# Kernel tuning notes

Measured on AMD Instinct MI355X. Metric: run time of the kernel, lower is better.

## Reference

```python
import jax, jax.numpy as jnp
import numpy as np

N_NODES = 100000
N_EDGES = 1600000
IN_DIM, HIDDEN, OUT_DIM = 128, 64, 32
LN_EPS = 1e-5


def setup_inputs() -> dict:
    key = jax.random.key(0)
    ks = jax.random.split(key, 12)
    x = jax.random.normal(ks[0], (N_NODES, IN_DIM), dtype=jnp.float32)
    edge_index = jax.random.randint(ks[1], (2, N_EDGES), 0, N_NODES, dtype=jnp.int64)
    s = 1.0 / np.sqrt(IN_DIM)
    s2 = 1.0 / np.sqrt(HIDDEN)
    return {
        "x": x,
        "edge_index": edge_index,
        "W_self0": jax.random.uniform(ks[2], (IN_DIM, HIDDEN), jnp.float32, -s, s),
        "W_neigh0": jax.random.uniform(ks[3], (IN_DIM, HIDDEN), jnp.float32, -s, s),
        "b0": jnp.zeros((HIDDEN,), jnp.float32),
        "g0": jnp.ones((HIDDEN,), jnp.float32),
        "be0": jnp.zeros((HIDDEN,), jnp.float32),
        "W_self1": jax.random.uniform(ks[4], (HIDDEN, OUT_DIM), jnp.float32, -s2, s2),
        "W_neigh1": jax.random.uniform(ks[5], (HIDDEN, OUT_DIM), jnp.float32, -s2, s2),
        "b1": jnp.zeros((OUT_DIM,), jnp.float32),
        "g1": jnp.ones((OUT_DIM,), jnp.float32),
        "be1": jnp.zeros((OUT_DIM,), jnp.float32),
    }


def _sage_layer(h, src, dst, W_self, W_neigh, b, g, be):
    n = h.shape[0]
    # mean aggregation of neighbor features via scatter-add + count
    agg = jax.ops.segment_sum(h[src], dst, num_segments=n)  # [N, F]
    cnt = jax.ops.segment_sum(jnp.ones((src.shape[0],), h.dtype), dst, num_segments=n)
    agg = agg / jnp.clip(cnt, 1.0)[:, None]
    z = h @ W_self + agg @ W_neigh + b  # [N, out]
    mu = jnp.mean(z, axis=-1, keepdims=True)
    var = jnp.mean((z - mu) ** 2, axis=-1, keepdims=True)
    zn = (z - mu) * jax.lax.rsqrt(var + LN_EPS) * g + be
    return jax.nn.relu(zn)


def reference(x, edge_index, W_self0, W_neigh0, b0, g0, be0,
              W_self1, W_neigh1, b1, g1, be1):
    src, dst = edge_index[0], edge_index[1]
    h = _sage_layer(x, src, dst, W_self0, W_neigh0, b0, g0, be0)
    h = _sage_layer(h, src, dst, W_self1, W_neigh1, b1, g1, be1)
    return h
```

## Files before the change

kernel.cpp:

```cpp
#include <hip/hip_runtime.h>
#include <hip/hip_bf16.h>

#define N_NODES 100000
#define N_EDGES 1600000
#define IN_DIM 128
#define HID 64
#define OUT_DIM 32
#define LN_EPS 1e-5f
#define NBKT 782
#define NPBLK 500
#define PAIRS_PER_BLK 1600
#define G0BLK 1563

typedef __attribute__((ext_vector_type(8))) _Float16 half8;
typedef __attribute__((ext_vector_type(4))) float f32x4;

__device__ __forceinline__ float uf(unsigned short u) {
  return __uint_as_float(((unsigned int)u) << 16);
}
__device__ __forceinline__ float uflo(unsigned int u) {
  return __uint_as_float(u << 16);
}
__device__ __forceinline__ float ufhi(unsigned int u) {
  return __uint_as_float(u & 0xffff0000u);
}
__device__ __forceinline__ unsigned short bf16rne(float f) {
  unsigned int u = __float_as_uint(f);
  unsigned int r = u + 0x7fffu + ((u >> 16) & 1u);
  return (unsigned short)(r >> 16);
}

__global__ void detect_edges(const int* __restrict__ w, int* __restrict__ flag) {
  __shared__ int any;
  if (threadIdx.x == 0) any = 0;
  __syncthreads();
  if (w[2 * threadIdx.x + 1] != 0) any = 1;
  __syncthreads();
  if (threadIdx.x == 0) flag[0] = any ? 0 : 1;
}

__global__ __launch_bounds__(256) void convW(
    const float* __restrict__ Wn0, const float* __restrict__ Ws0,
    const float* __restrict__ Wn1, const float* __restrict__ Ws1,
    _Float16* __restrict__ B0f, _Float16* __restrict__ B1f) {
  const int i = blockIdx.x * 256 + threadIdx.x;
  if (i < 128 * 128) {
    const int n = i >> 7, k = i & 127;
    const float w = (n < 64) ? Wn0[k * 64 + n] : Ws0[k * 64 + (n - 64)];
    B0f[i] = (_Float16)w;
  } else if (i < 128 * 128 + 64 * 64) {
    const int j = i - 128 * 128;
    const int n = j >> 6, k = j & 63;
    const float w = (n < 32) ? Wn1[k * 32 + n] : Ws1[k * 32 + (n - 32)];
    B1f[j] = (_Float16)w;
  }
}

__global__ __launch_bounds__(256) void g0pc(
    const float* __restrict__ x, const _Float16* __restrict__ B0f,
    const float* __restrict__ b0,
    unsigned short* __restrict__ p0u, float* __restrict__ s0b,
    const int* __restrict__ w, const int* __restrict__ flag,
    int* __restrict__ gcount, int* __restrict__ blkbase) {
  __shared__ _Float16 lb[128 * 128];
  const int tid = threadIdx.x;

  if (blockIdx.x < NPBLK) {
    int* h = (int*)lb;
    const int b = blockIdx.x;
    for (int i = tid; i < NBKT; i += 256) h[i] = 0;
    __syncthreads();
    const int i64 = flag[0];
    const int pEnd = (b + 1) * PAIRS_PER_BLK;
    for (int p = b * PAIRS_PER_BLK + tid; p < pEnd; p += 256) {
      int d0, d1;
      if (i64) {
        const int4 vd = *(const int4*)(w + 2 * (size_t)N_EDGES + 4 * (size_t)p);
        d0 = vd.x; d1 = vd.z;
      } else {
        const int2 vd = *(const int2*)(w + (size_t)N_EDGES + 2 * (size_t)p);
        d0 = vd.x; d1 = vd.y;
      }
      atomicAdd(&h[d0 >> 7], 1);
      atomicAdd(&h[d1 >> 7], 1);
    }
    __syncthreads();
    for (int i = tid; i < NBKT; i += 256)
      blkbase[b * NBKT + i] = atomicAdd(&gcount[i], h[i]);
    return;
  }

  {
    const uint4* gb = (const uint4*)B0f;
    for (int i = tid; i < 2048; i += 256) {
      const int o = i << 4;
      const int sw = o ^ (((o >> 8) & 7) << 4);
      *(uint4*)((char*)lb + sw) = gb[i];
    }
  }
  __syncthreads();
  const int lane = tid & 63;
  const int wave = tid >> 6;
  const int rowbase = (blockIdx.x - NPBLK) * 64 + wave * 16;
  const int arow = rowbase + (lane & 15);
  const int rclamp = (arow < N_NODES) ? arow : 0;
  const int ko = (lane >> 4) << 3;

  f32x4 acc[8];
#pragma unroll
  for (int ct = 0; ct < 8; ++ct) acc[ct] = (f32x4){0.f, 0.f, 0.f, 0.f};

  for (int ks = 0; ks < 4; ++ks) {
    float av[8];
    const float* ax = x + (size_t)rclamp * IN_DIM + ks * 32 + ko;
    *(float4*)&av[0] = *(const float4*)ax;
    *(float4*)&av[4] = *(const float4*)(ax + 4);
    half8 ah;
#pragma unroll
    for (int j = 0; j < 8; ++j) ah[j] = (_Float16)av[j];
    const int kb = ks * 64 + (ko << 1);
#pragma unroll
    for (int ct = 0; ct < 8; ++ct) {
      const int n = ct * 16 + (lane & 15);
      const int boff = (n << 8) + kb;
      const int sb = boff ^ (((boff >> 8) & 7) << 4);
      const half8 bv = *(const half8*)((const char*)lb + sb);
      acc[ct] = __builtin_amdgcn_mfma_f32_16x16x32_f16(ah, bv, acc[ct], 0, 0, 0);
    }
  }
  const int rb4 = rowbase + ((lane >> 4) << 2);
  const int cc = lane & 15;
#pragma unroll
  for (int ct = 0; ct < 4; ++ct) {
#pragma unroll
    for (int j = 0; j < 4; ++j) {
      const int r = rb4 + j;
      if (r < N_NODES) p0u[(size_t)r * HID + ct * 16 + cc] = bf16rne(acc[ct][j]);
    }
  }
#pragma unroll
  for (int ct = 4; ct < 8; ++ct) {
    const float bias = b0[(ct - 4) * 16 + cc];
#pragma unroll
    for (int j = 0; j < 4; ++j) {
      const int r = rb4 + j;
      if (r < N_NODES) s0b[(size_t)r * HID + (ct - 4) * 16 + cc] = acc[ct][j] + bias;
    }
  }
}

__global__ __launch_bounds__(256) void part_scan(
    const int* __restrict__ gcount, int* __restrict__ gbase) {
  __shared__ int lds[256];
  const int t = threadIdx.x;
  int v[4];
  int s = 0;
#pragma unroll
  for (int j = 0; j < 4; ++j) {
    const int idx = t * 4 + j;
    v[j] = (idx < NBKT) ? gcount[idx] : 0;
    s += v[j];
  }
  lds[t] = s;
  __syncthreads();
  for (int o = 1; o < 256; o <<= 1) {
    const int val = (t >= o) ? lds[t - o] : 0;
    __syncthreads();
    lds[t] += val;
    __syncthreads();
  }
  int run = lds[t] - s;
#pragma unroll
  for (int j = 0; j < 4; ++j) {
    const int idx = t * 4 + j;
    if (idx < NBKT) gbase[idx] = run;
    run += v[j];
  }
}

__global__ __launch_bounds__(256) void part_scatter(
    const int* __restrict__ w, const int* __restrict__ flag,
    const int* __restrict__ gbase, const int* __restrict__ blkbase,
    int2* __restrict__ pe) {
  __shared__ int cur[NBKT];
  const int t = threadIdx.x, b = blockIdx.x;
  for (int i = t; i < NBKT; i += 256)
    cur[i] = gbase[i] + blkbase[b * NBKT + i];
  __syncthreads();
  const int i64 = flag[0];
  const int pEnd = (b + 1) * PAIRS_PER_BLK;
  for (int p = b * PAIRS_PER_BLK + t; p < pEnd; p += 256) {
    int s0, s1, d0, d1;
    if (i64) {
      const int4 vs = *(const int4*)(w + 4 * (size_t)p);
      const int4 vd = *(const int4*)(w + 2 * (size_t)N_EDGES + 4 * (size_t)p);
      s0 = vs.x; s1 = vs.z;
      d0 = vd.x; d1 = vd.z;
    } else {
      const int2 vs = *(const int2*)(w + 2 * (size_t)p);
      const int2 vd = *(const int2*)(w + (size_t)N_EDGES + 2 * (size_t)p);
      s0 = vs.x; s1 = vs.y;
      d0 = vd.x; d1 = vd.y;
    }
    const int sl0 = atomicAdd(&cur[d0 >> 7], 1);
    pe[sl0] = make_int2(s0, d0);
    const int sl1 = atomicAdd(&cur[d1 >> 7], 1);
    pe[sl1] = make_int2(s1, d1);
  }
}

__global__ __launch_bounds__(256) void bucket_csr(
    const int2* __restrict__ pe, const int* __restrict__ gbase,
    const int* __restrict__ gcount, int* __restrict__ deg,
    int* __restrict__ off, int* __restrict__ sortedSrc) {
  __shared__ int ldeg[128];
  __shared__ int loff[128];
  __shared__ int lcur[128];
  const int t = threadIdx.x;
  const int bkt = blockIdx.x;
  const int nbase = bkt << 7;
  const int ebase = gbase[bkt];
  const int cnt = gcount[bkt];
  if (t < 128) ldeg[t] = 0;
  __syncthreads();
  for (int e = t; e < cnt; e += 256) {
    const int2 sd = pe[ebase + e];
    atomicAdd(&ldeg[sd.y - nbase], 1);
  }
  __syncthreads();
  if (t < 128) loff[t] = ldeg[t];
  __syncthreads();
  for (int o = 1; o < 128; o <<= 1) {
    int v = 0;
    if (t >= o && t < 128) v = loff[t - o];
    __syncthreads();
    if (t < 128) loff[t] += v;
    __syncthreads();
  }
  if (t < 128) {
    const int ex = loff[t] - ldeg[t];
    lcur[t] = ex;
    const int n = nbase + t;
    if (n < N_NODES) {
      deg[n] = ldeg[t];
      off[n] = ebase + ex;
    }
  }
  __syncthreads();
  for (int e = t; e < cnt; e += 256) {
    const int2 sd = pe[ebase + e];
    const int p = atomicAdd(&lcur[sd.y - nbase], 1);
    sortedSrc[ebase + p] = sd.x;
  }
}

__global__ __launch_bounds__(256) void gemm1(
    const float* __restrict__ h1, const _Float16* __restrict__ B1f,
    const float* __restrict__ b1,
    unsigned short* __restrict__ p1u, float* __restrict__ s1b) {
  __shared__ _Float16 lb[64 * 64];
  const int tid = threadIdx.x;
  {
    const uint4* gb = (const uint4*)B1f;
    for (int i = tid; i < 512; i += 256) {
      const int o = i << 4;
      const int sw = o ^ (((o >> 7) & 7) << 4);
      *(uint4*)((char*)lb + sw) = gb[i];
    }
  }
  __syncthreads();
  const int lane = tid & 63;
  const int wave = tid >> 6;
  const int rowbase = blockIdx.x * 64 + wave * 16;
  const int arow = rowbase + (lane & 15);
  const int rclamp = (arow < N_NODES) ? arow : 0;
  const int ko = (lane >> 4) << 3;

  f32x4 acc[4];
#pragma unroll
  for (int ct = 0; ct < 4; ++ct) acc[ct] = (f32x4){0.f, 0.f, 0.f, 0.f};

  for (int ks = 0; ks < 2; ++ks) {
    float av[8];
    const float* ax = h1 + (size_t)rclamp * HID + ks * 32 + ko;
    *(float4*)&av[0] = *(const float4*)ax;
    *(float4*)&av[4] = *(const float4*)(ax + 4);
    half8 ah;
#pragma unroll
    for (int j = 0; j < 8; ++j) ah[j] = (_Float16)av[j];
    const int kb = ks * 64 + (ko << 1);
#pragma unroll
    for (int ct = 0; ct < 4; ++ct) {
      const int n = ct * 16 + (lane & 15);
      const int boff = (n << 7) + kb;
      const int sb = boff ^ (((boff >> 7) & 7) << 4);
      const half8 bv = *(const half8*)((const char*)lb + sb);
      acc[ct] = __builtin_amdgcn_mfma_f32_16x16x32_f16(ah, bv, acc[ct], 0, 0, 0);
    }
  }
  const int rb4 = rowbase + ((lane >> 4) << 2);
  const int cc = lane & 15;
#pragma unroll
  for (int ct = 0; ct < 2; ++ct) {
#pragma unroll
    for (int j = 0; j < 4; ++j) {
      const int r = rb4 + j;
      if (r < N_NODES) p1u[(size_t)r * OUT_DIM + ct * 16 + cc] = bf16rne(acc[ct][j]);
    }
  }
#pragma unroll
  for (int ct = 2; ct < 4; ++ct) {
    const float bias = b1[(ct - 2) * 16 + cc];
#pragma unroll
    for (int j = 0; j < 4; ++j) {
      const int r = rb4 + j;
      if (r < N_NODES)
        s1b[(size_t)r * OUT_DIM + (ct - 2) * 16 + cc] = acc[ct][j] + bias;
    }
  }
}

__global__ __launch_bounds__(256) void aggc0(
    const int* __restrict__ sortedSrc, const int* __restrict__ off,
    const int* __restrict__ deg, const unsigned short* __restrict__ p0u,
    const float* __restrict__ s0b, const float* __restrict__ g,
    const float* __restrict__ be, float* __restrict__ h1) {
  const int lane = threadIdx.x & 63;
  const int h = lane >> 5;
  const int grp = (lane >> 3) & 3;
  const int sl = lane & 7;
  const int i = blockIdx.x * 8 + ((threadIdx.x >> 6) << 1) + h;
  const int st = off[i];
  const int dg = deg[i];
  const int dgmax = max(dg, __shfl_xor(dg, 32));
  float acc[8];
#pragma unroll
  for (int f = 0; f < 8; ++f) acc[f] = 0.f;

  for (int base = 0; base < dgmax; base += 32) {
    const int cnt = min(32, dg - base);
    const int l5 = lane & 31;
    const int idx = (l5 < cnt) ? sortedSrc[st + base + l5] : 0;
    const int cntmax = min(32, dgmax - base);
    for (int j = 0; j * 4 < cntmax; ++j) {
      const int e = j * 4 + grp;
      const float msk = (e < cnt) ? 1.f : 0.f;
      const int es = max(min(e, cnt - 1), 0);
      const int srcn = __shfl(idx, (h << 5) | es);
      const uint4 q = *(const uint4*)(p0u + (size_t)srcn * HID + sl * 8);
      acc[0] = fmaf(msk, uflo(q.x), acc[0]);
      acc[1] = fmaf(msk, ufhi(q.x), acc[1]);
      acc[2] = fmaf(msk, uflo(q.y), acc[2]);
      acc[3] = fmaf(msk, ufhi(q.y), acc[3]);
      acc[4] = fmaf(msk, uflo(q.z), acc[4]);
      acc[5] = fmaf(msk, ufhi(q.z), acc[5]);
      acc[6] = fmaf(msk, uflo(q.w), acc[6]);
      acc[7] = fmaf(msk, ufhi(q.w), acc[7]);
    }
  }
#pragma unroll
  for (int mk = 8; mk < 32; mk <<= 1) {
#pragma unroll
    for (int f = 0; f < 8; ++f) acc[f] += __shfl_xor(acc[f], mk);
  }
  const float inv = 1.0f / fmaxf((float)dg, 1.0f);
  float z[8];
  const float4 sb0 = *(const float4*)(s0b + (size_t)i * HID + sl * 8);
  const float4 sb1 = *(const float4*)(s0b + (size_t)i * HID + sl * 8 + 4);
  z[0] = sb0.x + acc[0] * inv; z[1] = sb0.y + acc[1] * inv;
  z[2] = sb0.z + acc[2] * inv; z[3] = sb0.w + acc[3] * inv;
  z[4] = sb1.x + acc[4] * inv; z[5] = sb1.y + acc[5] * inv;
  z[6] = sb1.z + acc[6] * inv; z[7] = sb1.w + acc[7] * inv;
  float pm = 0.f;
#pragma unroll
  for (int f = 0; f < 8; ++f) pm += z[f];
#pragma unroll
  for (int mk = 1; mk < 8; mk <<= 1) pm += __shfl_xor(pm, mk);
  const float mean = pm * (1.0f / 64.0f);
  float pv = 0.f;
#pragma unroll
  for (int f = 0; f < 8; ++f) {
    z[f] -= mean;
    pv += z[f] * z[f];
  }
#pragma unroll
  for (int mk = 1; mk < 8; mk <<= 1) pv += __shfl_xor(pv, mk);
  const float rstd = rsqrtf(pv * (1.0f / 64.0f) + LN_EPS);
  if (grp == 0) {
    const float4 gv0 = *(const float4*)(g + sl * 8);
    const float4 gv1 = *(const float4*)(g + sl * 8 + 4);
    const float4 bv0 = *(const float4*)(be + sl * 8);
    const float4 bv1 = *(const float4*)(be + sl * 8 + 4);
    float4 o0, o1;
    o0.x = fmaxf(z[0] * rstd * gv0.x + bv0.x, 0.f);
    o0.y = fmaxf(z[1] * rstd * gv0.y + bv0.y, 0.f);
    o0.z = fmaxf(z[2] * rstd * gv0.z + bv0.z, 0.f);
    o0.w = fmaxf(z[3] * rstd * gv0.w + bv0.w, 0.f);
    o1.x = fmaxf(z[4] * rstd * gv1.x + bv1.x, 0.f);
    o1.y = fmaxf(z[5] * rstd * gv1.y + bv1.y, 0.f);
    o1.z = fmaxf(z[6] * rstd * gv1.z + bv1.z, 0.f);
    o1.w = fmaxf(z[7] * rstd * gv1.w + bv1.w, 0.f);
    *(float4*)(h1 + (size_t)i * HID + sl * 8) = o0;
    *(float4*)(h1 + (size_t)i * HID + sl * 8 + 4) = o1;
  }
}

__global__ __launch_bounds__(256) void aggc1(
    const int* __restrict__ sortedSrc, const int* __restrict__ off,
    const int* __restrict__ deg, const unsigned short* __restrict__ p1u,
    const float* __restrict__ s1b, const float* __restrict__ g,
    const float* __restrict__ be, float* __restrict__ out) {
  const int lane = threadIdx.x & 63;
  const int q4 = lane >> 4;
  const int grp = (lane >> 2) & 3;
  const int sl = lane & 3;
  const int i = blockIdx.x * 16 + ((threadIdx.x >> 6) << 2) + q4;
  const int st = off[i];
  const int dg = deg[i];
  int dm = max(dg, __shfl_xor(dg, 16));
  const int dgmax = max(dm, __shfl_xor(dm, 32));
  float acc[8];
#pragma unroll
  for (int f = 0; f < 8; ++f) acc[f] = 0.f;

  for (int base = 0; base < dgmax; base += 16) {
    const int cnt = min(16, dg - base);
    const int l4 = lane & 15;
    const int idx = (l4 < cnt) ? sortedSrc[st + base + l4] : 0;
    const int cntmax = min(16, dgmax - base);
    for (int j = 0; j * 4 < cntmax; ++j) {
      const int e = j * 4 + grp;
      const float msk = (e < cnt) ? 1.f : 0.f;
      const int es = max(min(e, cnt - 1), 0);
      const int srcn = __shfl(idx, (q4 << 4) | es);
      const uint4 qv = *(const uint4*)(p1u + (size_t)srcn * OUT_DIM + sl * 8);
      acc[0] = fmaf(msk, uflo(qv.x), acc[0]);
      acc[1] = fmaf(msk, ufhi(qv.x), acc[1]);
      acc[2] = fmaf(msk, uflo(qv.y), acc[2]);
      acc[3] = fmaf(msk, ufhi(qv.y), acc[3]);
      acc[4] = fmaf(msk, uflo(qv.z), acc[4]);
      acc[5] = fmaf(msk, ufhi(qv.z), acc[5]);
      acc[6] = fmaf(msk, uflo(qv.w), acc[6]);
      acc[7] = fmaf(msk, ufhi(qv.w), acc[7]);
    }
  }
#pragma unroll
  for (int mk = 4; mk < 16; mk <<= 1) {
#pragma unroll
    for (int f = 0; f < 8; ++f) acc[f] += __shfl_xor(acc[f], mk);
  }
  const float inv = 1.0f / fmaxf((float)dg, 1.0f);
  float z[8];
  const float4 sb0 = *(const float4*)(s1b + (size_t)i * OUT_DIM + sl * 8);
  const float4 sb1 = *(const float4*)(s1b + (size_t)i * OUT_DIM + sl * 8 + 4);
  z[0] = sb0.x + acc[0] * inv; z[1] = sb0.y + acc[1] * inv;
  z[2] = sb0.z + acc[2] * inv; z[3] = sb0.w + acc[3] * inv;
  z[4] = sb1.x + acc[4] * inv; z[5] = sb1.y + acc[5] * inv;
  z[6] = sb1.z + acc[6] * inv; z[7] = sb1.w + acc[7] * inv;
  float pm = 0.f;
#pragma unroll
  for (int f = 0; f < 8; ++f) pm += z[f];
#pragma unroll
  for (int mk = 1; mk < 4; mk <<= 1) pm += __shfl_xor(pm, mk);
  const float mean = pm * (1.0f / 32.0f);
  float pv = 0.f;
#pragma unroll
  for (int f = 0; f < 8; ++f) {
    z[f] -= mean;
    pv += z[f] * z[f];
  }
#pragma unroll
  for (int mk = 1; mk < 4; mk <<= 1) pv += __shfl_xor(pv, mk);
  const float rstd = rsqrtf(pv * (1.0f / 32.0f) + LN_EPS);
  if (grp == 0) {
    const float4 gv0 = *(const float4*)(g + sl * 8);
    const float4 gv1 = *(const float4*)(g + sl * 8 + 4);
    const float4 bv0 = *(const float4*)(be + sl * 8);
    const float4 bv1 = *(const float4*)(be + sl * 8 + 4);
    float4 o0, o1;
    o0.x = fmaxf(z[0] * rstd * gv0.x + bv0.x, 0.f);
    o0.y = fmaxf(z[1] * rstd * gv0.y + bv0.y, 0.f);
    o0.z = fmaxf(z[2] * rstd * gv0.z + bv0.z, 0.f);
    o0.w = fmaxf(z[3] * rstd * gv0.w + bv0.w, 0.f);
    o1.x = fmaxf(z[4] * rstd * gv1.x + bv1.x, 0.f);
    o1.y = fmaxf(z[5] * rstd * gv1.y + bv1.y, 0.f);
    o1.z = fmaxf(z[6] * rstd * gv1.z + bv1.z, 0.f);
    o1.w = fmaxf(z[7] * rstd * gv1.w + bv1.w, 0.f);
    *(float4*)(out + (size_t)i * OUT_DIM + sl * 8) = o0;
    *(float4*)(out + (size_t)i * OUT_DIM + sl * 8 + 4) = o1;
  }
}

extern "C" void kernel_launch(void* const* d_in, const int* in_sizes, int n_in,
                              void* d_out, int out_size, void* d_ws, size_t ws_size,
                              hipStream_t stream) {
  const float* x       = (const float*)d_in[0];
  const int*   edges   = (const int*)d_in[1];
  const float* Wself0  = (const float*)d_in[2];
  const float* Wneigh0 = (const float*)d_in[3];
  const float* b0      = (const float*)d_in[4];
  const float* g0      = (const float*)d_in[5];
  const float* be0     = (const float*)d_in[6];
  const float* Wself1  = (const float*)d_in[7];
  const float* Wneigh1 = (const float*)d_in[8];
  const float* b1      = (const float*)d_in[9];
  const float* g1      = (const float*)d_in[10];
  const float* be1     = (const float*)d_in[11];

  int* flag      = (int*)d_ws;
  int* gcount    = flag + 64;
  int* gbase     = gcount + 1024;
  int* blkbase   = gbase + 1024;
  int* deg       = blkbase + 400000;
  int* off       = deg + N_NODES;
  int* sortedSrc = off + N_NODES;
  int2* pe       = (int2*)(sortedSrc + N_EDGES);
  _Float16* B0f  = (_Float16*)(pe + N_EDGES);
  _Float16* B1f  = B0f + 128 * 128;
  unsigned short* p0u = (unsigned short*)(B1f + 64 * 64);
  float* s0b = (float*)(p0u + (size_t)N_NODES * HID);
  float* h1  = s0b + (size_t)N_NODES * HID;
  unsigned short* p1u = p0u;
  float* s1b = s0b;

  hipMemsetAsync(gcount, 0, NBKT * sizeof(int), stream);

  detect_edges<<<1, 256, 0, stream>>>(edges, flag);
  convW<<<80, 256, 0, stream>>>(Wneigh0, Wself0, Wneigh1, Wself1, B0f, B1f);
  g0pc<<<NPBLK + G0BLK, 256, 0, stream>>>(x, B0f, b0, p0u, s0b,
                                          edges, flag, gcount, blkbase);
  part_scan<<<1, 256, 0, stream>>>(gcount, gbase);
  part_scatter<<<NPBLK, 256, 0, stream>>>(edges, flag, gbase, blkbase, pe);
  bucket_csr<<<NBKT, 256, 0, stream>>>(pe, gbase, gcount, deg, off, sortedSrc);

  aggc0<<<(N_NODES + 7) / 8, 256, 0, stream>>>(sortedSrc, off, deg, p0u, s0b,
                                               g0, be0, h1);
  gemm1<<<(N_NODES + 63) / 64, 256, 0, stream>>>(h1, B1f, b1, p1u, s1b);
  aggc1<<<(N_NODES + 15) / 16, 256, 0, stream>>>(sortedSrc, off, deg, p1u, s1b,
                                                 g1, be1, (float*)d_out);
}
```

Before: 161.3 us.

## Pad CSR rows to multiples of four with zero sentinel, pack edge pairs, split GEMM0 columns

Each node's neighbor list is padded to a multiple of four and the padding points at a zero-filled sentinel row, so the aggregation loops can drop the per-edge mask, clamp and FMA and just add. Partition entries are packed into one int (17-bit source plus 7-bit local destination) to halve the scatter and CSR traffic. GEMM0 is split into two column-group blocks, each using half the LDS and half the accumulators, which doubles the block count and should improve occupancy. The cost is extra padded gathers from the sentinel row, a larger workspace, and p1u now aliasing the pe buffer.

Measured after the change: 182.1 us. 13.0% more time.

```diff
diff --git a/kernel.cpp b/kernel.cpp
--- a/kernel.cpp
+++ b/kernel.cpp
@@ -10,14 +10,12 @@
 #define NBKT 782
 #define NPBLK 500
 #define PAIRS_PER_BLK 1600
-#define G0BLK 1563
+#define G0T 1563
+#define PADCAP 384
 
 typedef __attribute__((ext_vector_type(8))) _Float16 half8;
 typedef __attribute__((ext_vector_type(4))) float f32x4;
 
-__device__ __forceinline__ float uf(unsigned short u) {
-  return __uint_as_float(((unsigned int)u) << 16);
-}
 __device__ __forceinline__ float uflo(unsigned int u) {
   return __uint_as_float(u << 16);
 }
@@ -62,7 +60,7 @@
     unsigned short* __restrict__ p0u, float* __restrict__ s0b,
     const int* __restrict__ w, const int* __restrict__ flag,
     int* __restrict__ gcount, int* __restrict__ blkbase) {
-  __shared__ _Float16 lb[128 * 128];
+  __shared__ _Float16 lb[64 * 128];
   const int tid = threadIdx.x;
 
   if (blockIdx.x < NPBLK) {
@@ -90,25 +88,28 @@
     return;
   }
 
+  const int gb = blockIdx.x - NPBLK;
+  const int colgrp = (gb >= G0T) ? 1 : 0;
+  const int rowblk = colgrp ? (gb - G0T) : gb;
   {
-    const uint4* gb = (const uint4*)B0f;
-    for (int i = tid; i < 2048; i += 256) {
+    const uint4* gsrc = (const uint4*)(B0f + (colgrp << 13));
+    for (int i = tid; i < 1024; i += 256) {
       const int o = i << 4;
       const int sw = o ^ (((o >> 8) & 7) << 4);
-      *(uint4*)((char*)lb + sw) = gb[i];
+      *(uint4*)((char*)lb + sw) = gsrc[i];
     }
   }
   __syncthreads();
   const int lane = tid & 63;
   const int wave = tid >> 6;
-  const int rowbase = (blockIdx.x - NPBLK) * 64 + wave * 16;
+  const int rowbase = rowblk * 64 + wave * 16;
   const int arow = rowbase + (lane & 15);
   const int rclamp = (arow < N_NODES) ? arow : 0;
   const int ko = (lane >> 4) << 3;
 
-  f32x4 acc[8];
-#pragma unroll
-  for (int ct = 0; ct < 8; ++ct) acc[ct] = (f32x4){0.f, 0.f, 0.f, 0.f};
+  f32x4 acc[4];
+#pragma unroll
+  for (int ct = 0; ct < 4; ++ct) acc[ct] = (f32x4){0.f, 0.f, 0.f, 0.f};
 
   for (int ks = 0; ks < 4; ++ks) {
     float av[8];
@@ -120,7 +121,7 @@
     for (int j = 0; j < 8; ++j) ah[j] = (_Float16)av[j];
     const int kb = ks * 64 + (ko << 1);
 #pragma unroll
-    for (int ct = 0; ct < 8; ++ct) {
+    for (int ct = 0; ct < 4; ++ct) {
       const int n = ct * 16 + (lane & 15);
       const int boff = (n << 8) + kb;
       const int sb = boff ^ (((boff >> 8) & 7) << 4);
@@ -130,21 +131,24 @@
   }
   const int rb4 = rowbase + ((lane >> 4) << 2);
   const int cc = lane & 15;
-#pragma unroll
-  for (int ct = 0; ct < 4; ++ct) {
-#pragma unroll
-    for (int j = 0; j < 4; ++j) {
-      const int r = rb4 + j;
-      if (r < N_NODES) p0u[(size_t)r * HID + ct * 16 + cc] = bf16rne(acc[ct][j]);
-    }
-  }
-#pragma unroll
-  for (int ct = 4; ct < 8; ++ct) {
-    const float bias = b0[(ct - 4) * 16 + cc];
-#pragma unroll
-    for (int j = 0; j < 4; ++j) {
-      const int r = rb4 + j;
-      if (r < N_NODES) s0b[(size_t)r * HID + (ct - 4) * 16 + cc] = acc[ct][j] + bias;
+  if (colgrp == 0) {
+#pragma unroll
+    for (int ct = 0; ct < 4; ++ct) {
+#pragma unroll
+      for (int j = 0; j < 4; ++j) {
+        const int r = rb4 + j;
+        if (r < N_NODES) p0u[(size_t)r * HID + ct * 16 + cc] = bf16rne(acc[ct][j]);
+      }
+    }
+  } else {
+#pragma unroll
+    for (int ct = 0; ct < 4; ++ct) {
+      const float bias = b0[ct * 16 + cc];
+#pragma unroll
+      for (int j = 0; j < 4; ++j) {
+        const int r = rb4 + j;
+        if (r < N_NODES) s0b[(size_t)r * HID + ct * 16 + cc] = acc[ct][j] + bias;
+      }
     }
   }
 }
@@ -181,7 +185,7 @@
 __global__ __launch_bounds__(256) void part_scatter(
     const int* __restrict__ w, const int* __restrict__ flag,
     const int* __restrict__ gbase, const int* __restrict__ blkbase,
-    int2* __restrict__ pe) {
+    int* __restrict__ pe) {
   __shared__ int cur[NBKT];
   const int t = threadIdx.x, b = blockIdx.x;
   for (int i = t; i < NBKT; i += 256)
@@ -203,14 +207,14 @@
       d0 = vd.x; d1 = vd.y;
     }
     const int sl0 = atomicAdd(&cur[d0 >> 7], 1);
-    pe[sl0] = make_int2(s0, d0);
+    pe[sl0] = s0 | ((d0 & 127) << 17);
     const int sl1 = atomicAdd(&cur[d1 >> 7], 1);
-    pe[sl1] = make_int2(s1, d1);
+    pe[sl1] = s1 | ((d1 & 127) << 17);
   }
 }
 
 __global__ __launch_bounds__(256) void bucket_csr(
-    const int2* __restrict__ pe, const int* __restrict__ gbase,
+    const int* __restrict__ pe, const int* __restrict__ gbase,
     const int* __restrict__ gcount, int* __restrict__ deg,
     int* __restrict__ off, int* __restrict__ sortedSrc) {
   __shared__ int ldeg[128];
@@ -221,14 +225,15 @@
   const int nbase = bkt << 7;
   const int ebase = gbase[bkt];
   const int cnt = gcount[bkt];
+  const int outbase = ebase + PADCAP * bkt;
   if (t < 128) ldeg[t] = 0;
   __syncthreads();
   for (int e = t; e < cnt; e += 256) {
-    const int2 sd = pe[ebase + e];
-    atomicAdd(&ldeg[sd.y - nbase], 1);
-  }
-  __syncthreads();
-  if (t < 128) loff[t] = ldeg[t];
+    const int pv = pe[ebase + e];
+    atomicAdd(&ldeg[(pv >> 17) & 127], 1);
+  }
+  __syncthreads();
+  if (t < 128) loff[t] = (ldeg[t] + 3) & ~3;
   __syncthreads();
   for (int o = 1; o < 128; o <<= 1) {
     int v = 0;
@@ -238,19 +243,28 @@
     __syncthreads();
   }
   if (t < 128) {
-    const int ex = loff[t] - ldeg[t];
+    const int pdeg = (ldeg[t] + 3) & ~3;
+    const int ex = loff[t] - pdeg;
     lcur[t] = ex;
     const int n = nbase + t;
     if (n < N_NODES) {
       deg[n] = ldeg[t];
-      off[n] = ebase + ex;
+      off[n] = outbase + ex;
     }
   }
   __syncthreads();
   for (int e = t; e < cnt; e += 256) {
-    const int2 sd = pe[ebase + e];
-    const int p = atomicAdd(&lcur[sd.y - nbase], 1);
-    sortedSrc[ebase + p] = sd.x;
+    const int pv = pe[ebase + e];
+    const int ld = (pv >> 17) & 127;
+    const int p = atomicAdd(&lcur[ld], 1);
+    sortedSrc[outbase + p] = pv & 0x1FFFF;
+  }
+  __syncthreads();
+  if (t < 128) {
+    const int pdeg = (ldeg[t] + 3) & ~3;
+    const int ex = loff[t] - pdeg;
+    for (int q = ldeg[t]; q < pdeg; ++q)
+      sortedSrc[outbase + ex + q] = N_NODES;
   }
 }
 
@@ -332,30 +346,25 @@
   const int i = blockIdx.x * 8 + ((threadIdx.x >> 6) << 1) + h;
   const int st = off[i];
   const int dg = deg[i];
-  const int dgmax = max(dg, __shfl_xor(dg, 32));
+  const int dgp = (dg + 3) & ~3;
+  const int dgmaxp = max(dgp, __shfl_xor(dgp, 32));
   float acc[8];
 #pragma unroll
   for (int f = 0; f < 8; ++f) acc[f] = 0.f;
 
-  for (int base = 0; base < dgmax; base += 32) {
-    const int cnt = min(32, dg - base);
+  for (int base = 0; base < dgmaxp; base += 32) {
+    const int cntp = dgp - base;
     const int l5 = lane & 31;
-    const int idx = (l5 < cnt) ? sortedSrc[st + base + l5] : 0;
-    const int cntmax = min(32, dgmax - base);
-    for (int j = 0; j * 4 < cntmax; ++j) {
+    const int idx = (l5 < cntp) ? sortedSrc[st + base + l5] : N_NODES;
+    const int cm = min(32, dgmaxp - base);
+    for (int j = 0; j * 4 < cm; ++j) {
       const int e = j * 4 + grp;
-      const float msk = (e < cnt) ? 1.f : 0.f;
-      const int es = max(min(e, cnt - 1), 0);
-      const int srcn = __shfl(idx, (h << 5) | es);
+      const int srcn = __shfl(idx, (h << 5) | e);
       const uint4 q = *(const uint4*)(p0u + (size_t)srcn * HID + sl * 8);
-      acc[0] = fmaf(msk, uflo(q.x), acc[0]);
-      acc[1] = fmaf(msk, ufhi(q.x), acc[1]);
-      acc[2] = fmaf(msk, uflo(q.y), acc[2]);
-      acc[3] = fmaf(msk, ufhi(q.y), acc[3]);
-      acc[4] = fmaf(msk, uflo(q.z), acc[4]);
-      acc[5] = fmaf(msk, ufhi(q.z), acc[5]);
-      acc[6] = fmaf(msk, uflo(q.w), acc[6]);
-      acc[7] = fmaf(msk, ufhi(q.w), acc[7]);
+      acc[0] += uflo(q.x); acc[1] += ufhi(q.x);
+      acc[2] += uflo(q.y); acc[3] += ufhi(q.y);
+      acc[4] += uflo(q.z); acc[5] += ufhi(q.z);
+      acc[6] += uflo(q.w); acc[7] += ufhi(q.w);
     }
   }
 #pragma unroll
@@ -417,31 +426,26 @@
   const int i = blockIdx.x * 16 + ((threadIdx.x >> 6) << 2) + q4;
   const int st = off[i];
   const int dg = deg[i];
-  int dm = max(dg, __shfl_xor(dg, 16));
-  const int dgmax = max(dm, __shfl_xor(dm, 32));
+  const int dgp = (dg + 3) & ~3;
+  int dm = max(dgp, __shfl_xor(dgp, 16));
+  const int dgmaxp = max(dm, __shfl_xor(dm, 32));
   float acc[8];
 #pragma unroll
   for (int f = 0; f < 8; ++f) acc[f] = 0.f;
 
-  for (int base = 0; base < dgmax; base += 16) {
-    const int cnt = min(16, dg - base);
+  for (int base = 0; base < dgmaxp; base += 16) {
+    const int cntp = dgp - base;
     const int l4 = lane & 15;
-    const int idx = (l4 < cnt) ? sortedSrc[st + base + l4] : 0;
-    const int cntmax = min(16, dgmax - base);
-    for (int j = 0; j * 4 < cntmax; ++j) {
+    const int idx = (l4 < cntp) ? sortedSrc[st + base + l4] : N_NODES;
+    const int cm = min(16, dgmaxp - base);
+    for (int j = 0; j * 4 < cm; ++j) {
       const int e = j * 4 + grp;
-      const float msk = (e < cnt) ? 1.f : 0.f;
-      const int es = max(min(e, cnt - 1), 0);
-      const int srcn = __shfl(idx, (q4 << 4) | es);
+      const int srcn = __shfl(idx, (q4 << 4) | e);
       const uint4 qv = *(const uint4*)(p1u + (size_t)srcn * OUT_DIM + sl * 8);
-      acc[0] = fmaf(msk, uflo(qv.x), acc[0]);
-      acc[1] = fmaf(msk, ufhi(qv.x), acc[1]);
-      acc[2] = fmaf(msk, uflo(qv.y), acc[2]);
-      acc[3] = fmaf(msk, ufhi(qv.y), acc[3]);
-      acc[4] = fmaf(msk, uflo(qv.z), acc[4]);
-      acc[5] = fmaf(msk, ufhi(qv.z), acc[5]);
-      acc[6] = fmaf(msk, uflo(qv.w), acc[6]);
-      acc[7] = fmaf(msk, ufhi(qv.w), acc[7]);
+      acc[0] += uflo(qv.x); acc[1] += ufhi(qv.x);
+      acc[2] += uflo(qv.y); acc[3] += ufhi(qv.y);
+      acc[4] += uflo(qv.z); acc[5] += ufhi(qv.z);
+      acc[6] += uflo(qv.w); acc[7] += ufhi(qv.w);
     }
   }
 #pragma unroll
@@ -514,28 +518,33 @@
   int* deg       = blkbase + 400000;
   int* off       = deg + N_NODES;
   int* sortedSrc = off + N_NODES;
-  int2* pe       = (int2*)(sortedSrc + N_EDGES);
-  _Float16* B0f  = (_Float16*)(pe + N_EDGES);
+  int* pe        = sortedSrc + 1950000;
+  _Float16* B0f  = (_Float16*)(pe + 1620000);
   _Float16* B1f  = B0f + 128 * 128;
   unsigned short* p0u = (unsigned short*)(B1f + 64 * 64);
-  float* s0b = (float*)(p0u + (size_t)N_NODES * HID);
+  float* s0b = (float*)(p0u + ((size_t)N_NODES + 1) * HID);
   float* h1  = s0b + (size_t)N_NODES * HID;
-  unsigned short* p1u = p0u;
+  unsigned short* p1u = (unsigned short*)pe;
   float* s1b = s0b;
 
   hipMemsetAsync(gcount, 0, NBKT * sizeof(int), stream);
+  hipMemsetAsync(p0u + (size_t)N_NODES * HID, 0, HID * sizeof(unsigned short),
+                 stream);
 
   detect_edges<<<1, 256, 0, stream>>>(edges, flag);
   convW<<<80, 256, 0, stream>>>(Wneigh0, Wself0, Wneigh1, Wself1, B0f, B1f);
-  g0pc<<<NPBLK + G0BLK, 256, 0, stream>>>(x, B0f, b0, p0u, s0b,
-                                          edges, flag, gcount, blkbase);
+  g0pc<<<NPBLK + 2 * G0T, 256, 0, stream>>>(x, B0f, b0, p0u, s0b,
+                                            edges, flag, gcount, blkbase);
   part_scan<<<1, 256, 0, stream>>>(gcount, gbase);
   part_scatter<<<NPBLK, 256, 0, stream>>>(edges, flag, gbase, blkbase, pe);
   bucket_csr<<<NBKT, 256, 0, stream>>>(pe, gbase, gcount, deg, off, sortedSrc);
 
-  aggc0<<<(N_NODES + 7) / 8, 256, 0, stream>>>(sortedSrc, off, deg, p0u, s0b,
-                                               g0, be0, h1);
+  hipMemsetAsync(p1u + (size_t)N_NODES * OUT_DIM, 0,
+                 OUT_DIM * sizeof(unsigned short), stream);
+
+  aggc0<<<N_NODES / 8, 256, 0, stream>>>(sortedSrc, off, deg, p0u, s0b,
+                                         g0, be0, h1);
   gemm1<<<(N_NODES + 63) / 64, 256, 0, stream>>>(h1, B1f, b1, p1u, s1b);
-  aggc1<<<(N_NODES + 15) / 16, 256, 0, stream>>>(sortedSrc, off, deg, p1u, s1b,
-                                                 g1, be1, (float*)d_out);
-}
+  aggc1<<<N_NODES / 16, 256, 0, stream>>>(sortedSrc, off, deg, p1u, s1b,
+                                          g1, be1, (float*)d_out);
+}
```
